# Optimization experiments

Hardware: AMD Instinct MI355X
Metric: run time of the kernel (lower is better)

## Reference

```python
import jax, jax.numpy as jnp
import numpy as np

N = 100000
D = 128
A = 4096          # num_anchors
S = 512           # num_samples per anchor
NUM_CLASSES = 10
TEMP = 0.1


def setup_inputs() -> dict:
    key = jax.random.key(0)
    k1, k2, k3, k4 = jax.random.split(key, 4)
    x = jax.random.normal(k1, (N, D), dtype=jnp.float32)
    y = jax.random.randint(k2, (N,), 0, NUM_CLASSES)
    anchors = jax.random.randint(k3, (A,), 0, N)
    sampled = jax.random.randint(k4, (A, S), 0, N)
    return {"x": x, "y": y, "anchors": anchors, "sampled": sampled}


def reference(x, y, anchors, sampled):
    # L2-normalize once; cosine similarity then reduces to a dot product.
    xn = x / jnp.linalg.norm(x, axis=-1, keepdims=True)          # [N, D]
    a_feat = xn[anchors]                                          # [A, D]
    s_feat = xn[sampled]                                          # [A, S, D]
    sim = jnp.einsum('ad,asd->as', a_feat, s_feat)                # [A, S]
    e = jnp.exp(sim / TEMP)                                       # [A, S]
    pos_mask = (y[sampled] == y[anchors][:, None]).astype(e.dtype)  # [A, S]
    numerator = jnp.sum(e * pos_mask, axis=-1)                    # [A]
    denominator = jnp.sum(e, axis=-1)                             # [A]
    cnt = jnp.sum(pos_mask, axis=-1)                              # [A] positives per anchor
    safe_cnt = jnp.maximum(cnt, 1.0)
    safe_num = jnp.where(cnt > 0, numerator, 1.0)
    per_anchor = -jnp.log(safe_num / denominator) / safe_cnt      # [A]
    per_anchor = jnp.where(cnt > 0, per_anchor, 0.0)
    return jnp.sum(per_anchor)
```

## Files before the change

kernel.cpp:

```cpp
#include <hip/hip_runtime.h>
#include <math.h>

#define DIM 128
#define TEMP_INV 10.0f
#define LOG2E 1.4426950408889634f
#define QSCALE 20.0f
#define NCLASS 16
#define C0 (TEMP_INV * LOG2E / (QSCALE * QSCALE))

#if __has_builtin(__builtin_amdgcn_udot8)
#define UDOT8(a, b, c) __builtin_amdgcn_udot8((a), (b), (c), false)
#else
static __device__ __forceinline__ unsigned udot8_sw(unsigned a, unsigned b, unsigned c) {
#pragma unroll
    for (int i = 0; i < 8; ++i)
        c += ((a >> (4 * i)) & 15u) * ((b >> (4 * i)) & 15u);
    return c;
}
#define UDOT8(a, b, c) udot8_sw((a), (b), (c))
#endif

__global__ __launch_bounds__(256) void norm_i4_kernel(const float* __restrict__ x,
                                                      unsigned short* __restrict__ xq,
                                                      float* __restrict__ out,
                                                      int N) {
    if (blockIdx.x == 0 && threadIdx.x == 0) out[0] = 0.0f;
    int lane = threadIdx.x & 31;
    int grp  = threadIdx.x >> 5;
    int row  = blockIdx.x * 8 + grp;
    if (row >= N) return;
    float4 v = *(const float4*)(x + (size_t)row * DIM + lane * 4);
    float s = v.x*v.x + v.y*v.y + v.z*v.z + v.w*v.w;
    s += __shfl_xor(s, 16); s += __shfl_xor(s, 8); s += __shfl_xor(s, 4);
    s += __shfl_xor(s, 2);  s += __shfl_xor(s, 1);
    float inv = rsqrtf(s) * QSCALE;
    int q0 = (int)fminf(fmaxf(rintf(v.x * inv), -7.0f), 7.0f) + 8;
    int q1 = (int)fminf(fmaxf(rintf(v.y * inv), -7.0f), 7.0f) + 8;
    int q2 = (int)fminf(fmaxf(rintf(v.z * inv), -7.0f), 7.0f) + 8;
    int q3 = (int)fminf(fmaxf(rintf(v.w * inv), -7.0f), 7.0f) + 8;
    xq[(size_t)row * 32 + lane] = (unsigned short)(q0 | (q1 << 4) | (q2 << 8) | (q3 << 12));
}

__global__ __launch_bounds__(256) void bitmap_kernel(const int* __restrict__ y,
                                                     unsigned int* __restrict__ bitmap,
                                                     int words, int N,
                                                     float* __restrict__ partials, int A3) {
    int gtid = blockIdx.x * 256 + threadIdx.x;
    if (gtid < A3) partials[gtid] = 0.0f;

    int wave = threadIdx.x >> 6;
    int lane = threadIdx.x & 63;
    int base = blockIdx.x * 256 + wave * 64;
    if (base >= N) return;
    int n  = base + lane;
    int yv = (n < N) ? (y[n] & (NCLASS - 1)) : 255;
    int w0 = base >> 5;
#pragma unroll
    for (int c = 0; c < NCLASS; ++c) {
        unsigned long long m = __ballot(yv == c);
        if (lane == 0) {
            bitmap[(size_t)c * words + w0] = (unsigned int)m;
            if (w0 + 1 < words)
                bitmap[(size_t)c * words + w0 + 1] = (unsigned int)(m >> 32);
        }
    }
}

__global__ __launch_bounds__(256, 8) void loss_i4_kernel(const unsigned int* __restrict__ xq,
                                                         const int* __restrict__ y,
                                                         const int* __restrict__ anchors,
                                                         const int* __restrict__ sampled,
                                                         const unsigned int* __restrict__ bitmap,
                                                         int words,
                                                         float* __restrict__ p_num,
                                                         float* __restrict__ p_den,
                                                         float* __restrict__ p_cnt,
                                                         int S) {
    int a    = blockIdx.x >> 1;
    int q    = blockIdx.x & 1;
    int tid  = threadIdx.x;
    int wave = tid >> 6;
    int lane = tid & 63;
    int g    = lane >> 2;
    int k    = lane & 3;

    __shared__ __align__(16) char stage[4 * 4096];
    __shared__ int s_pk[256];

    int anchor = anchors[a];
    int ya     = y[anchor] & (NCLASS - 1);
    const unsigned int* bm = bitmap + (size_t)ya * words;

    const int* samp = sampled + (size_t)a * S + (size_t)q * 256;
    {
        int si  = samp[tid];
        int pos = (bm[si >> 5] >> (si & 31)) & 1;
        s_pk[tid] = (si << 1) | pos;
    }

    uint4 an = *(const uint4*)(xq + (size_t)anchor * 16 + k * 4);
    int Ta;
    {
        unsigned t = 0;
        t = UDOT8(an.x, 0x11111111u, t);
        t = UDOT8(an.y, 0x11111111u, t);
        t = UDOT8(an.z, 0x11111111u, t);
        t = UDOT8(an.w, 0x11111111u, t);
        int ti = (int)t;
        ti += __shfl_xor(ti, 1); ti += __shfl_xor(ti, 2);
        Ta = ti;
    }
    __syncthreads();

    const char* xqb = (const char*)xq;
    char* wavebuf = stage + wave * 4096;
#pragma unroll
    for (int b = 0; b < 4; ++b) {
        int idx = s_pk[wave * 64 + b * 16 + (lane >> 2)] >> 1;
        const void* gp = xqb + (size_t)idx * 64 + (lane & 3) * 16;
        __builtin_amdgcn_global_load_lds((const __attribute__((address_space(1))) void*)gp,
                                         (__attribute__((address_space(3))) void*)(wavebuf + b * 1024),
                                         16, 0, 0);
    }
    asm volatile("s_waitcnt vmcnt(0)" ::: "memory");

    float num = 0.0f, den = 0.0f, cnt = 0.0f;
#pragma unroll
    for (int b = 0; b < 4; ++b) {
        int pk = s_pk[wave * 64 + b * 16 + g];
        const uint4 sr = *(const uint4*)(wavebuf + b * 1024 + g * 64 + k * 16);
        unsigned bb = 0, ts = 0;
        bb = UDOT8(sr.x, an.x, bb);  ts = UDOT8(sr.x, 0x11111111u, ts);
        bb = UDOT8(sr.y, an.y, bb);  ts = UDOT8(sr.y, 0x11111111u, ts);
        bb = UDOT8(sr.z, an.z, bb);  ts = UDOT8(sr.z, 0x11111111u, ts);
        bb = UDOT8(sr.w, an.w, bb);  ts = UDOT8(sr.w, 0x11111111u, ts);
        int c = (int)bb - 8 * (int)ts;
        c += __shfl_xor(c, 1); c += __shfl_xor(c, 2);
        int dint = c - 8 * Ta + 8192;
        float e = exp2f((float)dint * C0);
        den += e;
        bool pos = (pk & 1);
        num += pos ? e : 0.0f;  cnt += pos ? 1.0f : 0.0f;
    }

    num += __shfl_xor(num, 4);  den += __shfl_xor(den, 4);  cnt += __shfl_xor(cnt, 4);
    num += __shfl_xor(num, 8);  den += __shfl_xor(den, 8);  cnt += __shfl_xor(cnt, 8);
    num += __shfl_xor(num, 16); den += __shfl_xor(den, 16); cnt += __shfl_xor(cnt, 16);
    num += __shfl_xor(num, 32); den += __shfl_xor(den, 32); cnt += __shfl_xor(cnt, 32);
    if (lane == 0) {
        atomicAdd(p_num + a, num);
        atomicAdd(p_den + a, den);
        atomicAdd(p_cnt + a, cnt);
    }
}

__global__ __launch_bounds__(256) void finalize_kernel(const float* __restrict__ p_num,
                                                       const float* __restrict__ p_den,
                                                       const float* __restrict__ p_cnt,
                                                       float* __restrict__ out,
                                                       int A) {
    int a = blockIdx.x * 256 + threadIdx.x;
    float loss = 0.0f;
    if (a < A) {
        float tc = p_cnt[a];
        if (tc > 0.0f) loss = -__logf(p_num[a] / p_den[a]) / tc;
    }
    loss += __shfl_xor(loss, 1);  loss += __shfl_xor(loss, 2);
    loss += __shfl_xor(loss, 4);  loss += __shfl_xor(loss, 8);
    loss += __shfl_xor(loss, 16); loss += __shfl_xor(loss, 32);
    if ((threadIdx.x & 63) == 0) atomicAdd(out, loss);
}


__global__ __launch_bounds__(256) void norm_kernel(const float* __restrict__ x,
                                                   float* __restrict__ inv_norm,
                                                   float* __restrict__ out,
                                                   int N) {
    if (blockIdx.x == 0 && threadIdx.x == 0) out[0] = 0.0f;
    int wave = threadIdx.x >> 6;
    int lane = threadIdx.x & 63;
    int row  = blockIdx.x * 4 + wave;
    if (row >= N) return;
    const float2 v = *(const float2*)(x + (size_t)row * DIM + lane * 2);
    float s = v.x * v.x + v.y * v.y;
    s += __shfl_xor(s, 32); s += __shfl_xor(s, 16); s += __shfl_xor(s, 8);
    s += __shfl_xor(s, 4);  s += __shfl_xor(s, 2);  s += __shfl_xor(s, 1);
    if (lane == 0) inv_norm[row] = rsqrtf(s);
}

__global__ __launch_bounds__(256) void loss_kernel(const float* __restrict__ x,
                                                   const int* __restrict__ y,
                                                   const int* __restrict__ anchors,
                                                   const int* __restrict__ sampled,
                                                   const float* __restrict__ inv_norm,
                                                   float* __restrict__ out,
                                                   int S) {
    int a     = blockIdx.x;
    int tid   = threadIdx.x;
    int lane  = tid & 31;
    int group = tid >> 5;

    int   anchor = anchors[a];
    int   ya     = y[anchor];
    float inv_a  = inv_norm[anchor];
    float4 av = *(const float4*)(x + (size_t)anchor * DIM + lane * 4);
    av.x *= inv_a; av.y *= inv_a; av.z *= inv_a; av.w *= inv_a;

    float num = 0.0f, den = 0.0f, cnt = 0.0f;
    const int* samp = sampled + (size_t)a * S;

#pragma unroll 4
    for (int s = group; s < S; s += 8) {
        int   sidx  = samp[s];
        float inv_s = inv_norm[sidx];
        int   ys    = y[sidx];
        const float4 sv = *(const float4*)(x + (size_t)sidx * DIM + lane * 4);
        float d = av.x * sv.x + av.y * sv.y + av.z * sv.z + av.w * sv.w;
        d += __shfl_xor(d, 16); d += __shfl_xor(d, 8); d += __shfl_xor(d, 4);
        d += __shfl_xor(d, 2);  d += __shfl_xor(d, 1);
        float e = __expf(d * inv_s * TEMP_INV);
        den += e;
        bool pos = (ys == ya);
        num += pos ? e : 0.0f;
        cnt += pos ? 1.0f : 0.0f;
    }

    __shared__ float s_num[8], s_den[8], s_cnt[8];
    if (lane == 0) { s_num[group] = num; s_den[group] = den; s_cnt[group] = cnt; }
    __syncthreads();
    if (tid == 0) {
        float tn = 0.0f, td = 0.0f, tc = 0.0f;
        for (int g = 0; g < 8; ++g) { tn += s_num[g]; td += s_den[g]; tc += s_cnt[g]; }
        float loss = 0.0f;
        if (tc > 0.0f) loss = -__logf(tn / td) / tc;
        atomicAdd(out, loss);
    }
}

extern "C" void kernel_launch(void* const* d_in, const int* in_sizes, int n_in,
                              void* d_out, int out_size, void* d_ws, size_t ws_size,
                              hipStream_t stream) {
    const float* x       = (const float*)d_in[0];
    const int*   y       = (const int*)d_in[1];
    const int*   anchors = (const int*)d_in[2];
    const int*   sampled = (const int*)d_in[3];

    int N = in_sizes[1];
    int A = in_sizes[2];
    int S = in_sizes[3] / A;

    float* out = (float*)d_out;
    int words = (N + 31) / 32;
    size_t off_bm = (size_t)N * 64;
    size_t off_pp = off_bm + (size_t)NCLASS * words * 4;
    size_t need   = off_pp + (size_t)3 * A * sizeof(float);

    if (ws_size >= need && S == 512) {
        unsigned short* xq4    = (unsigned short*)d_ws;
        unsigned int*   bitmap = (unsigned int*)((char*)d_ws + off_bm);
        float*          part   = (float*)((char*)d_ws + off_pp);
        float* p_num = part;
        float* p_den = part + A;
        float* p_cnt = part + 2 * A;

        norm_i4_kernel<<<(N + 7) / 8, 256, 0, stream>>>(x, xq4, out, N);
        bitmap_kernel<<<(N + 255) / 256, 256, 0, stream>>>(y, bitmap, words, N,
                                                           part, 3 * A);
        loss_i4_kernel<<<A * 2, 256, 0, stream>>>((const unsigned int*)xq4, y, anchors,
                                                  sampled, bitmap, words,
                                                  p_num, p_den, p_cnt, S);
        finalize_kernel<<<(A + 255) / 256, 256, 0, stream>>>(p_num, p_den, p_cnt, out, A);
    } else {
        float* inv_norm = (float*)d_ws;
        norm_kernel<<<(N + 3) / 4, 256, 0, stream>>>(x, inv_norm, out, N);
        loss_kernel<<<A, 256, 0, stream>>>(x, y, anchors, sampled, inv_norm, out, S);
    }
}
```

Measured before the change: 128.8 us.

## Bin sampled pairs by feature block and sweep blocks from LDS

Replaces the per-anchor gather of sampled rows with a scatter that bins every (anchor, sample) pair by 1024-row feature block and anchor group. A sweep kernel then stages each 64KB block of quantized features into LDS and computes each pair's exp-similarity from there, writing into a per-pair buffer; bins that exceed their capacity spill to an overflow list handled by a single block. A final per-anchor kernel reduces num/den/count and the loss. The goal is to turn random 64-byte gathers into streaming reads, at the cost of global atomics for binning, extra kernels and writing then re-reading a 2M-entry intermediate.

```diff
diff --git a/kernel.cpp b/kernel.cpp
--- a/kernel.cpp
+++ b/kernel.cpp
@@ -7,6 +7,9 @@
 #define QSCALE 20.0f
 #define NCLASS 16
 #define C0 (TEMP_INV * LOG2E / (QSCALE * QSCALE))
+#define ONES 0x11111111u
+#define CAP 80
+#define OVF_MAX 4096
 
 #if __has_builtin(__builtin_amdgcn_udot8)
 #define UDOT8(a, b, c) __builtin_amdgcn_udot8((a), (b), (c), false)
@@ -19,6 +22,7 @@
 }
 #define UDOT8(a, b, c) udot8_sw((a), (b), (c))
 #endif
+
 
 __global__ __launch_bounds__(256) void norm_i4_kernel(const float* __restrict__ x,
                                                       unsigned short* __restrict__ xq,
@@ -44,9 +48,9 @@
 __global__ __launch_bounds__(256) void bitmap_kernel(const int* __restrict__ y,
                                                      unsigned int* __restrict__ bitmap,
                                                      int words, int N,
-                                                     float* __restrict__ partials, int A3) {
+                                                     unsigned int* __restrict__ zbuf, int zn) {
     int gtid = blockIdx.x * 256 + threadIdx.x;
-    if (gtid < A3) partials[gtid] = 0.0f;
+    if (gtid < zn) zbuf[gtid] = 0u;
 
     int wave = threadIdx.x >> 6;
     int lane = threadIdx.x & 63;
@@ -66,109 +70,153 @@
     }
 }
 
-__global__ __launch_bounds__(256, 8) void loss_i4_kernel(const unsigned int* __restrict__ xq,
-                                                         const int* __restrict__ y,
-                                                         const int* __restrict__ anchors,
-                                                         const int* __restrict__ sampled,
-                                                         const unsigned int* __restrict__ bitmap,
-                                                         int words,
-                                                         float* __restrict__ p_num,
-                                                         float* __restrict__ p_den,
-                                                         float* __restrict__ p_cnt,
-                                                         int S) {
-    int a    = blockIdx.x >> 1;
-    int q    = blockIdx.x & 1;
+__global__ __launch_bounds__(256) void aq_kernel(const unsigned int* __restrict__ xq,
+                                                 const int* __restrict__ anchors,
+                                                 unsigned int* __restrict__ aq, int A16) {
+    int t = blockIdx.x * 256 + threadIdx.x;
+    if (t >= A16) return;
+    int a = t >> 4, w = t & 15;
+    aq[t] = xq[(size_t)anchors[a] * 16 + w];
+}
+
+__global__ __launch_bounds__(256) void scatter_kernel(const int* __restrict__ sampled,
+                                                      unsigned int* __restrict__ cnt,
+                                                      unsigned int* __restrict__ recs,
+                                                      unsigned int* __restrict__ ovf_c,
+                                                      unsigned long long* __restrict__ ovf,
+                                                      int total) {
+    int t = blockIdx.x * 256 + threadIdx.x;
+    if (t >= total) return;
+    int idx = sampled[t];
+    int a   = t >> 9;
+    int bin = (idx >> 10) * 512 + (a >> 3);
+    unsigned pos = atomicAdd(cnt + bin, 1u);
+    if (pos < CAP) {
+        recs[(size_t)bin * CAP + pos] = ((unsigned)(idx & 1023) << 21) | (unsigned)t;
+    } else {
+        unsigned o = atomicAdd(ovf_c, 1u);
+        if (o < OVF_MAX) ovf[o] = ((unsigned long long)(unsigned)idx << 32) | (unsigned)t;
+    }
+}
+
+__global__ __launch_bounds__(512) void sweep_kernel(const unsigned int* __restrict__ xq,
+                                                    const unsigned int* __restrict__ aq,
+                                                    const unsigned int* __restrict__ cnt,
+                                                    const unsigned int* __restrict__ recs,
+                                                    float* __restrict__ e_out, int N) {
+    __shared__ __align__(16) char stage[65536];
+    int bucket = blockIdx.x >> 3;
+    int sub    = blockIdx.x & 7;
     int tid  = threadIdx.x;
     int wave = tid >> 6;
     int lane = tid & 63;
-    int g    = lane >> 2;
-    int k    = lane & 3;
-
-    __shared__ __align__(16) char stage[4 * 4096];
-    __shared__ int s_pk[256];
-
+
+    const char* xqb   = (const char*)xq;
+    size_t base  = (size_t)bucket << 16;
+    size_t limit = (size_t)N << 6;
+#pragma unroll
+    for (int r = 0; r < 8; ++r) {
+        int o = r * 8192 + wave * 1024 + lane * 16;
+        size_t gb = base + (size_t)o;
+        if (gb < limit) {
+            __builtin_amdgcn_global_load_lds((const __attribute__((address_space(1))) void*)(xqb + gb),
+                                             (__attribute__((address_space(3))) void*)(stage + r * 8192 + wave * 1024),
+                                             16, 0, 0);
+        }
+    }
+    asm volatile("s_waitcnt vmcnt(0)" ::: "memory");
+    __syncthreads();
+
+    int g = tid >> 2, k = tid & 3;
+    int binL = g & 63, par = g >> 6;
+    int bin = bucket * 512 + sub * 64 + binL;
+    int cn = (int)cnt[bin];
+    if (cn > CAP) cn = CAP;
+    const unsigned int* rb = recs + (size_t)bin * CAP;
+    for (int it = par; it < cn; it += 2) {
+        unsigned rec = rb[it];
+        int slot = (int)(rec & 0x1FFFFFu);
+        int lidx = (int)(rec >> 21);
+        int a    = slot >> 9;
+        const uint4 sr = *(const uint4*)(stage + (lidx << 6) + (k << 4));
+        const uint4 an = *(const uint4*)(aq + (size_t)a * 16 + k * 4);
+        unsigned bb = 0, t1 = 0, t2 = 0;
+        bb = UDOT8(sr.x, an.x, bb);  t1 = UDOT8(sr.x, ONES, t1);  t2 = UDOT8(an.x, ONES, t2);
+        bb = UDOT8(sr.y, an.y, bb);  t1 = UDOT8(sr.y, ONES, t1);  t2 = UDOT8(an.y, ONES, t2);
+        bb = UDOT8(sr.z, an.z, bb);  t1 = UDOT8(sr.z, ONES, t1);  t2 = UDOT8(an.z, ONES, t2);
+        bb = UDOT8(sr.w, an.w, bb);  t1 = UDOT8(sr.w, ONES, t1);  t2 = UDOT8(an.w, ONES, t2);
+        int pc = (int)bb - 8 * (int)(t1 + t2);
+        pc += __shfl_xor(pc, 1); pc += __shfl_xor(pc, 2);
+        if (k == 0) e_out[slot] = exp2f((float)(pc + 8192) * C0);
+    }
+}
+
+__global__ __launch_bounds__(256) void ovf_kernel(const unsigned int* __restrict__ xq,
+                                                  const unsigned int* __restrict__ aq,
+                                                  const unsigned int* __restrict__ ovf_c,
+                                                  const unsigned long long* __restrict__ ovf,
+                                                  float* __restrict__ e_out) {
+    unsigned n = *ovf_c;
+    if (n > OVF_MAX) n = OVF_MAX;
+    int g = threadIdx.x >> 2, k = threadIdx.x & 3;
+    for (unsigned j = g; j < n; j += 64) {
+        unsigned long long r = ovf[j];
+        int idx  = (int)(r >> 32);
+        int slot = (int)(r & 0xFFFFFFFFu);
+        int a    = slot >> 9;
+        const uint4 sr = *(const uint4*)(xq + (size_t)idx * 16 + k * 4);
+        const uint4 an = *(const uint4*)(aq + (size_t)a * 16 + k * 4);
+        unsigned bb = 0, t1 = 0, t2 = 0;
+        bb = UDOT8(sr.x, an.x, bb);  t1 = UDOT8(sr.x, ONES, t1);  t2 = UDOT8(an.x, ONES, t2);
+        bb = UDOT8(sr.y, an.y, bb);  t1 = UDOT8(sr.y, ONES, t1);  t2 = UDOT8(an.y, ONES, t2);
+        bb = UDOT8(sr.z, an.z, bb);  t1 = UDOT8(sr.z, ONES, t1);  t2 = UDOT8(an.z, ONES, t2);
+        bb = UDOT8(sr.w, an.w, bb);  t1 = UDOT8(sr.w, ONES, t1);  t2 = UDOT8(an.w, ONES, t2);
+        int pc = (int)bb - 8 * (int)(t1 + t2);
+        pc += __shfl_xor(pc, 1); pc += __shfl_xor(pc, 2);
+        if (k == 0) e_out[slot] = exp2f((float)(pc + 8192) * C0);
+    }
+}
+
+__global__ __launch_bounds__(256) void reduce_kernel(const float* __restrict__ e_out,
+                                                     const int* __restrict__ y,
+                                                     const int* __restrict__ anchors,
+                                                     const int* __restrict__ sampled,
+                                                     const unsigned int* __restrict__ bitmap,
+                                                     int words,
+                                                     float* __restrict__ out) {
+    int a = blockIdx.x, t = threadIdx.x;
     int anchor = anchors[a];
     int ya     = y[anchor] & (NCLASS - 1);
     const unsigned int* bm = bitmap + (size_t)ya * words;
-
-    const int* samp = sampled + (size_t)a * S + (size_t)q * 256;
-    {
-        int si  = samp[tid];
-        int pos = (bm[si >> 5] >> (si & 31)) & 1;
-        s_pk[tid] = (si << 1) | pos;
-    }
-
-    uint4 an = *(const uint4*)(xq + (size_t)anchor * 16 + k * 4);
-    int Ta;
-    {
-        unsigned t = 0;
-        t = UDOT8(an.x, 0x11111111u, t);
-        t = UDOT8(an.y, 0x11111111u, t);
-        t = UDOT8(an.z, 0x11111111u, t);
-        t = UDOT8(an.w, 0x11111111u, t);
-        int ti = (int)t;
-        ti += __shfl_xor(ti, 1); ti += __shfl_xor(ti, 2);
-        Ta = ti;
-    }
+    float num = 0.0f, den = 0.0f, cntf = 0.0f;
+#pragma unroll
+    for (int h = 0; h < 2; ++h) {
+        int slot = (a << 9) + t + h * 256;
+        float e  = e_out[slot];
+        int si   = sampled[slot];
+        int pos  = (bm[si >> 5] >> (si & 31)) & 1;
+        den += e;
+        num += pos ? e : 0.0f;
+        cntf += (float)pos;
+    }
+    num += __shfl_xor(num, 1);  den += __shfl_xor(den, 1);  cntf += __shfl_xor(cntf, 1);
+    num += __shfl_xor(num, 2);  den += __shfl_xor(den, 2);  cntf += __shfl_xor(cntf, 2);
+    num += __shfl_xor(num, 4);  den += __shfl_xor(den, 4);  cntf += __shfl_xor(cntf, 4);
+    num += __shfl_xor(num, 8);  den += __shfl_xor(den, 8);  cntf += __shfl_xor(cntf, 8);
+    num += __shfl_xor(num, 16); den += __shfl_xor(den, 16); cntf += __shfl_xor(cntf, 16);
+    num += __shfl_xor(num, 32); den += __shfl_xor(den, 32); cntf += __shfl_xor(cntf, 32);
+    __shared__ float sn[4], sd[4], sc[4];
+    int wv = t >> 6;
+    if ((t & 63) == 0) { sn[wv] = num; sd[wv] = den; sc[wv] = cntf; }
     __syncthreads();
-
-    const char* xqb = (const char*)xq;
-    char* wavebuf = stage + wave * 4096;
-#pragma unroll
-    for (int b = 0; b < 4; ++b) {
-        int idx = s_pk[wave * 64 + b * 16 + (lane >> 2)] >> 1;
-        const void* gp = xqb + (size_t)idx * 64 + (lane & 3) * 16;
-        __builtin_amdgcn_global_load_lds((const __attribute__((address_space(1))) void*)gp,
-                                         (__attribute__((address_space(3))) void*)(wavebuf + b * 1024),
-                                         16, 0, 0);
-    }
-    asm volatile("s_waitcnt vmcnt(0)" ::: "memory");
-
-    float num = 0.0f, den = 0.0f, cnt = 0.0f;
-#pragma unroll
-    for (int b = 0; b < 4; ++b) {
-        int pk = s_pk[wave * 64 + b * 16 + g];
-        const uint4 sr = *(const uint4*)(wavebuf + b * 1024 + g * 64 + k * 16);
-        unsigned bb = 0, ts = 0;
-        bb = UDOT8(sr.x, an.x, bb);  ts = UDOT8(sr.x, 0x11111111u, ts);
-        bb = UDOT8(sr.y, an.y, bb);  ts = UDOT8(sr.y, 0x11111111u, ts);
-        bb = UDOT8(sr.z, an.z, bb);  ts = UDOT8(sr.z, 0x11111111u, ts);
-        bb = UDOT8(sr.w, an.w, bb);  ts = UDOT8(sr.w, 0x11111111u, ts);
-        int c = (int)bb - 8 * (int)ts;
-        c += __shfl_xor(c, 1); c += __shfl_xor(c, 2);
-        int dint = c - 8 * Ta + 8192;
-        float e = exp2f((float)dint * C0);
-        den += e;
-        bool pos = (pk & 1);
-        num += pos ? e : 0.0f;  cnt += pos ? 1.0f : 0.0f;
-    }
-
-    num += __shfl_xor(num, 4);  den += __shfl_xor(den, 4);  cnt += __shfl_xor(cnt, 4);
-    num += __shfl_xor(num, 8);  den += __shfl_xor(den, 8);  cnt += __shfl_xor(cnt, 8);
-    num += __shfl_xor(num, 16); den += __shfl_xor(den, 16); cnt += __shfl_xor(cnt, 16);
-    num += __shfl_xor(num, 32); den += __shfl_xor(den, 32); cnt += __shfl_xor(cnt, 32);
-    if (lane == 0) {
-        atomicAdd(p_num + a, num);
-        atomicAdd(p_den + a, den);
-        atomicAdd(p_cnt + a, cnt);
-    }
-}
-
-__global__ __launch_bounds__(256) void finalize_kernel(const float* __restrict__ p_num,
-                                                       const float* __restrict__ p_den,
-                                                       const float* __restrict__ p_cnt,
-                                                       float* __restrict__ out,
-                                                       int A) {
-    int a = blockIdx.x * 256 + threadIdx.x;
-    float loss = 0.0f;
-    if (a < A) {
-        float tc = p_cnt[a];
-        if (tc > 0.0f) loss = -__logf(p_num[a] / p_den[a]) / tc;
-    }
-    loss += __shfl_xor(loss, 1);  loss += __shfl_xor(loss, 2);
-    loss += __shfl_xor(loss, 4);  loss += __shfl_xor(loss, 8);
-    loss += __shfl_xor(loss, 16); loss += __shfl_xor(loss, 32);
-    if ((threadIdx.x & 63) == 0) atomicAdd(out, loss);
+    if (t == 0) {
+        float tn = sn[0] + sn[1] + sn[2] + sn[3];
+        float td = sd[0] + sd[1] + sd[2] + sd[3];
+        float tc = sc[0] + sc[1] + sc[2] + sc[3];
+        float loss = 0.0f;
+        if (tc > 0.0f) loss = -__logf(tn / td) / tc;
+        atomicAdd(out, loss);
+    }
 }
 
 
@@ -251,25 +299,40 @@
 
     float* out = (float*)d_out;
     int words = (N + 31) / 32;
-    size_t off_bm = (size_t)N * 64;
-    size_t off_pp = off_bm + (size_t)NCLASS * words * 4;
-    size_t need   = off_pp + (size_t)3 * A * sizeof(float);
-
-    if (ws_size >= need && S == 512) {
-        unsigned short* xq4    = (unsigned short*)d_ws;
-        unsigned int*   bitmap = (unsigned int*)((char*)d_ws + off_bm);
-        float*          part   = (float*)((char*)d_ws + off_pp);
-        float* p_num = part;
-        float* p_den = part + A;
-        float* p_cnt = part + 2 * A;
-
+    int NB    = (N + 1023) >> 10;
+    int NBIN  = NB * 512;
+
+    size_t off_bm   = (size_t)N * 64;
+    size_t off_aq   = off_bm + (size_t)NCLASS * words * 4;
+    size_t off_cnt  = off_aq + (size_t)A * 64;
+    size_t off_ovfc = off_cnt + (size_t)NBIN * 4;
+    size_t off_ovf  = off_ovfc + 8;
+    size_t off_rec  = off_ovf + (size_t)OVF_MAX * 8;
+    size_t off_e    = off_rec + (size_t)NBIN * CAP * 4;
+    size_t need     = off_e + (size_t)A * S * 4;
+
+    if (ws_size >= need && S == 512 && A <= 4096) {
+        unsigned short*     xq4    = (unsigned short*)d_ws;
+        const unsigned int* xqw    = (const unsigned int*)d_ws;
+        unsigned int*       bitmap = (unsigned int*)((char*)d_ws + off_bm);
+        unsigned int*       aq     = (unsigned int*)((char*)d_ws + off_aq);
+        unsigned int*       cnt    = (unsigned int*)((char*)d_ws + off_cnt);
+        unsigned int*       ovfc   = (unsigned int*)((char*)d_ws + off_ovfc);
+        unsigned long long* ovf    = (unsigned long long*)((char*)d_ws + off_ovf);
+        unsigned int*       recs   = (unsigned int*)((char*)d_ws + off_rec);
+        float*              e_out  = (float*)((char*)d_ws + off_e);
+
+        int total = A * S;
         norm_i4_kernel<<<(N + 7) / 8, 256, 0, stream>>>(x, xq4, out, N);
         bitmap_kernel<<<(N + 255) / 256, 256, 0, stream>>>(y, bitmap, words, N,
-                                                           part, 3 * A);
-        loss_i4_kernel<<<A * 2, 256, 0, stream>>>((const unsigned int*)xq4, y, anchors,
-                                                  sampled, bitmap, words,
-                                                  p_num, p_den, p_cnt, S);
-        finalize_kernel<<<(A + 255) / 256, 256, 0, stream>>>(p_num, p_den, p_cnt, out, A);
+                                                           cnt, NBIN + 2);
+        aq_kernel<<<(A * 16 + 255) / 256, 256, 0, stream>>>(xqw, anchors, aq, A * 16);
+        scatter_kernel<<<(total + 255) / 256, 256, 0, stream>>>(sampled, cnt, recs,
+                                                                ovfc, ovf, total);
+        sweep_kernel<<<NB * 8, 512, 0, stream>>>(xqw, aq, cnt, recs, e_out, N);
+        ovf_kernel<<<1, 256, 0, stream>>>(xqw, aq, ovfc, ovf, e_out);
+        reduce_kernel<<<A, 256, 0, stream>>>(e_out, y, anchors, sampled, bitmap,
+                                             words, out);
     } else {
         float* inv_norm = (float*)d_ws;
         norm_kernel<<<(N + 3) / 4, 256, 0, stream>>>(x, inv_norm, out, N);
```

Result: slower. 305.2 us (+136.9%).
